# Kernel tuning notes

Hardware: AMD Instinct MI355X
Metric: run time of the kernel (lower is better)

Reference implementation:

```python
import jax, jax.numpy as jnp
import numpy as np

DIM = 1024
TOPK = 64
PAIRS = DIM // 2  # phase_pairs default
PHASE_MIX = 0.5
GATE_THRESHOLD = 0.0
EPS = 1e-12  # F.normalize default eps


def _l2norm(v):
    # matches F.normalize(v, dim=-1): v / max(||v||, eps)
    n = jnp.linalg.norm(v, axis=-1, keepdims=True)
    return v / jnp.maximum(n, EPS)


def setup_inputs() -> dict:
    key = jax.random.key(0)
    ks = jax.random.split(key, 6)
    s = 0.02  # small init scale for weights
    return {
        "x": jax.random.normal(ks[0], (4, 4096, DIM), dtype=jnp.float32),
        "gate_W": jax.random.normal(ks[1], (DIM, DIM), dtype=jnp.float32) * s,
        "gate_b": jnp.zeros((DIM,), dtype=jnp.float32),
        "mag_W": jax.random.normal(ks[2], (DIM, DIM), dtype=jnp.float32) * s,
        "mag_b": jnp.zeros((DIM,), dtype=jnp.float32),
        "Wq": jax.random.normal(ks[3], (DIM, DIM), dtype=jnp.float32) * s,
        "Wk": jax.random.normal(ks[4], (DIM, DIM), dtype=jnp.float32) * s,
        "phase_W": jax.random.normal(ks[5], (2 * PAIRS, DIM), dtype=jnp.float32) * s,
    }


def reference(x, gate_W, gate_b, mag_W, mag_b, Wq, Wk, phase_W):
    B, S, D = x.shape
    # gated SAE-style projection (gated=True, diag=False)
    gate_pre = x @ gate_W.T + gate_b          # [B,S,D]
    mag_pre = x @ mag_W.T + mag_b             # [B,S,D]
    # hard gate with straight-through estimator
    gate_soft = jax.nn.sigmoid(gate_pre)
    gate_hard = (gate_pre > GATE_THRESHOLD).astype(x.dtype)
    gate = gate_hard + gate_soft - jax.lax.stop_gradient(gate_soft)
    mag = jax.nn.relu(mag_pre)
    # top-k scatter mask along feature dim
    idx = jax.lax.top_k(gate_pre, TOPK)[1]    # [B,S,K]
    rows = jnp.arange(B * S)[:, None]
    mask = (jnp.zeros((B * S, D), dtype=bool)
            .at[rows, idx.reshape(B * S, TOPK)].set(True)
            .reshape(B, S, D))
    gate = jnp.where(mask, gate, jnp.zeros_like(gate))
    mag = jnp.where(mask, mag, jnp.zeros_like(mag))
    xg = gate * mag
    # twist projections, L2-normalized
    q = _l2norm(xg @ Wq.T)
    k = _l2norm(xg @ Wk.T)
    # symplectic momentum map over consecutive steps
    momentum_map = q[:, 1:] * k[:, :-1] - q[:, :-1] * k[:, 1:]  # [B,S-1,D]
    twist_mag = jnp.linalg.norm(momentum_map, axis=-1, keepdims=True)
    complexity = jnp.pad(jnp.tanh(twist_mag), ((0, 0), (1, 0), (0, 0)))  # [B,S,1]
    # phase branch (phase_mix > 0)
    phase = (xg @ phase_W.T).reshape(B, S, PAIRS, 2)
    phase = _l2norm(phase)
    pp, pc = phase[:, :-1], phase[:, 1:]
    cross = pp[..., 0] * pc[..., 1] - pp[..., 1] * pc[..., 0]   # [B,S-1,P]
    dot = jnp.clip(jnp.sum(pp * pc, axis=-1), -1.0, 1.0)
    phase_delta = jnp.abs(jnp.arctan2(cross, dot)) / jnp.pi
    phase_score = jnp.pad(jnp.mean(phase_delta, axis=-1, keepdims=True),
                          ((0, 0), (1, 0), (0, 0)))             # [B,S,1]
    return (1.0 - PHASE_MIX) * complexity + PHASE_MIX * phase_score
```

## Files before the change

### kernel.cpp

```cpp
#include <hip/hip_runtime.h>
#include <math.h>

#define DIM 1024
#define ROWS 16384
#define SEQ 4096
#define MARGIN 0.012f
#define MAXC 24

typedef __bf16 v8bf __attribute__((ext_vector_type(8)));
typedef float v4f __attribute__((ext_vector_type(4)));
typedef int v8i __attribute__((ext_vector_type(8)));

__device__ __forceinline__ unsigned short f2bf(float f){
  unsigned u = __float_as_uint(f);
  u = u + 0x7FFFu + ((u >> 16) & 1u);
  return (unsigned short)(u >> 16);
}
__device__ __forceinline__ float bf2f(unsigned short h){
  return __uint_as_float(((unsigned)h) << 16);
}
__device__ __forceinline__ unsigned short relu_bf(unsigned short h){
  return (h & 0x8000u) ? (unsigned short)0 : h;
}
__device__ __forceinline__ unsigned f2fp8(float f){
  float a = fabsf(f);
  unsigned sign = (__float_as_uint(f) >> 24) & 0x80u;
  if (a >= 448.f) return sign | 0x7Eu;
  if (a < 0.015625f){
    int k = (int)rintf(a * 512.f);
    if (k >= 8) return sign | 0x08u;
    return sign | (unsigned)k;
  }
  unsigned u = __float_as_uint(a);
  u += 0x7FFFFu + ((u >> 20) & 1u);
  int e = (int)((u >> 23) & 0xFFu) - 127;
  unsigned m = (u >> 20) & 7u;
  if (e > 8) return sign | 0x7Eu;
  return sign | ((unsigned)(e + 7) << 3) | m;
}
__device__ __forceinline__ void lds_fence(){
  __asm__ volatile("s_waitcnt lgkmcnt(0)" ::: "memory");
}

__global__ __launch_bounds__(256) void cvt_all(
    const float* __restrict__ x,
    const float* __restrict__ w0, const float* __restrict__ w1,
    const float* __restrict__ w2, const float* __restrict__ w3,
    const float* __restrict__ w4,
    unsigned short* __restrict__ xbf, unsigned short* __restrict__ wbf,
    unsigned char* __restrict__ wf8){
  const int y = blockIdx.y;
  int i = (blockIdx.x * 256 + threadIdx.x) * 4;
  if (y < 16){
    const float* s = x + ((size_t)y << 20);
    float4 f = *(const float4*)(s + i);
    ushort4 o; o.x = f2bf(f.x); o.y = f2bf(f.y); o.z = f2bf(f.z); o.w = f2bf(f.w);
    *(ushort4*)(xbf + ((size_t)y << 20) + i) = o;
  } else if (y < 18){
    const float* s = (y == 16) ? w0 : w1;
    float4 f = *(const float4*)(s + i);
    ushort4 o; o.x = f2bf(f.x); o.y = f2bf(f.y); o.z = f2bf(f.z); o.w = f2bf(f.w);
    *(ushort4*)(wbf + ((size_t)(y - 16) << 20) + i) = o;
  } else {
    const float* s = (y == 18) ? w2 : ((y == 19) ? w3 : w4);
    float4 f = *(const float4*)(s + i);
    unsigned u = f2fp8(f.x * 32.f) | (f2fp8(f.y * 32.f) << 8) |
                 (f2fp8(f.z * 32.f) << 16) | (f2fp8(f.w * 32.f) << 24);
    *(unsigned*)(wf8 + ((size_t)(y - 18) << 20) + i) = u;
  }
}

#define GBAR() asm volatile("s_barrier" ::: "memory")
#define GLGKM0() { asm volatile("s_waitcnt lgkmcnt(0)" ::: "memory"); __builtin_amdgcn_sched_barrier(0); }
#define GVM4() asm volatile("s_waitcnt vmcnt(4)" ::: "memory")

__global__ __launch_bounds__(512, 2) void gemm_bt(
    const unsigned short* __restrict__ A, const unsigned short* __restrict__ B,
    const float* __restrict__ bias0, const float* __restrict__ bias1,
    unsigned short* __restrict__ C0, unsigned short* __restrict__ C1)
{
  extern __shared__ unsigned char lds[];
  const int t = threadIdx.x;
  const int lane = t & 63, wave = t >> 6;
  const int wr = wave >> 2, wc = wave & 3;
  const int bid = blockIdx.x;
  const int swz = (bid & 7) * 64 + (bid >> 3);
  const int m0 = (swz & 63) * 256;
  const int n0 = (swz >> 6) * 256;

  int offv[4];
#pragma unroll
  for (int h = 0; h < 2; h++)
#pragma unroll
    for (int i = 0; i < 2; i++){
      int o = h * 16384 + i * 8192 + t * 16;
      int u = o ^ (((o >> 9) & 1) << 5);
      int r = ((u >> 11) << 4) | ((u >> 6) & 15);
      int c = (((u >> 10) & 1) << 5) | ((u & 63) >> 1);
      offv[h * 2 + i] = r * 1024 + c;
    }
  const int off00 = offv[0], off01 = offv[1], off10 = offv[2], off11 = offv[3];
  const unsigned short* Ab = A + ((size_t)m0 << 10);
  const unsigned short* Bb = B + ((size_t)n0 << 10);

  const int laneterm = (lane & 15) * 64 + (((lane >> 4) * 16) ^ (((lane >> 3) & 1) * 32));
  const int aBase = wr * 16384 + laneterm;
  const int bBase = 32768 + wc * 8192 + laneterm;

#define GLD1(srcp, dsto) __builtin_amdgcn_global_load_lds( \
    (const __attribute__((address_space(1))) void*)(srcp), \
    (__attribute__((address_space(3))) void*)(lds + (dsto)), 16, 0, 0)

  auto stageA = [&](int h, int kt, int pp){
    const int o0 = h ? off10 : off00, o1 = h ? off11 : off01;
    GLD1(Ab + o0 + kt * 64, pp * 65536 + h * 16384 + t * 16);
    GLD1(Ab + o1 + kt * 64, pp * 65536 + h * 16384 + 8192 + t * 16);
  };
  auto stageB = [&](int h, int kt, int pp){
    const int o0 = h ? off10 : off00, o1 = h ? off11 : off01;
    GLD1(Bb + o0 + kt * 64, pp * 65536 + 32768 + h * 16384 + t * 16);
    GLD1(Bb + o1 + kt * 64, pp * 65536 + 32768 + h * 16384 + 8192 + t * 16);
  };

  v4f acc[8][4];
#pragma unroll
  for (int i = 0; i < 8; i++)
#pragma unroll
    for (int j = 0; j < 4; j++) acc[i][j] = v4f{0.f, 0.f, 0.f, 0.f};

  stageB(0, 0, 0); stageB(1, 0, 0);
  stageA(0, 0, 0); stageA(1, 0, 0);
  stageB(0, 1, 1); stageB(1, 1, 1);
  GVM4();
  GBAR();

  int p = 0;
  for (int X = 0; X < 16; X++, p ^= 1){
    const int pb = p * 65536;
    const int ktA = (X + 1 < 16) ? X + 1 : 15;
    const int ktB = (X + 2 < 16) ? X + 2 : X;
    v8bf a0[8], a1[8], b0[4], b1[4];

#pragma unroll
    for (int mi = 0; mi < 8; mi++) a0[mi] = *(const v8bf*)(lds + pb + aBase + mi * 2048);
#pragma unroll
    for (int ni = 0; ni < 4; ni++) b0[ni] = *(const v8bf*)(lds + pb + bBase + ni * 2048);
    stageA(0, ktA, p ^ 1);
    GBAR();
    __builtin_amdgcn_s_setprio(1);
#pragma unroll
    for (int mi = 0; mi < 4; mi++)
#pragma unroll
      for (int ni = 0; ni < 4; ni++)
        acc[mi][ni] = __builtin_amdgcn_mfma_f32_16x16x32_bf16(a0[mi], b0[ni], acc[mi][ni], 0, 0, 0);
    __builtin_amdgcn_s_setprio(0);
    GBAR();

#pragma unroll
    for (int mi = 0; mi < 4; mi++) a1[mi] = *(const v8bf*)(lds + pb + aBase + 1024 + mi * 2048);
#pragma unroll
    for (int ni = 0; ni < 4; ni++) b1[ni] = *(const v8bf*)(lds + pb + bBase + 1024 + ni * 2048);
    stageA(1, ktA, p ^ 1);
    GBAR();
    __builtin_amdgcn_s_setprio(1);
#pragma unroll
    for (int mi = 0; mi < 4; mi++)
#pragma unroll
      for (int ni = 0; ni < 4; ni++)
        acc[4 + mi][ni] = __builtin_amdgcn_mfma_f32_16x16x32_bf16(a0[4 + mi], b0[ni], acc[4 + mi][ni], 0, 0, 0);
    __builtin_amdgcn_s_setprio(0);
    GLGKM0();
    GBAR();

#pragma unroll
    for (int mi = 4; mi < 8; mi++) a1[mi] = *(const v8bf*)(lds + pb + aBase + 1024 + mi * 2048);
    stageB(0, ktB, p);
    GBAR();
    __builtin_amdgcn_s_setprio(1);
#pragma unroll
    for (int mi = 0; mi < 4; mi++)
#pragma unroll
      for (int ni = 0; ni < 4; ni++)
        acc[mi][ni] = __builtin_amdgcn_mfma_f32_16x16x32_bf16(a1[mi], b1[ni], acc[mi][ni], 0, 0, 0);
    __builtin_amdgcn_s_setprio(0);
    GBAR();

    stageB(1, ktB, p);
    GBAR();
    __builtin_amdgcn_s_setprio(1);
#pragma unroll
    for (int mi = 0; mi < 4; mi++)
#pragma unroll
      for (int ni = 0; ni < 4; ni++)
        acc[4 + mi][ni] = __builtin_amdgcn_mfma_f32_16x16x32_bf16(a1[4 + mi], b1[ni], acc[4 + mi][ni], 0, 0, 0);
    __builtin_amdgcn_s_setprio(0);
    GVM4();
    GBAR();
  }

  asm volatile("s_waitcnt vmcnt(0)" ::: "memory");
  __syncthreads();

  const int os = n0 >> 10;
  unsigned short* Cp = (os == 0) ? C0 : C1;
  const float* bp = (os == 0) ? bias0 : bias1;
  const int colbase = n0 & (DIM - 1);
  unsigned short* lt = (unsigned short*)lds;
  const int ar = lane & 15, aq = lane >> 4;
  const int lrw = wr * 16 + aq * 4;
  const int lrow = t >> 4;
  const int cseg = (t & 15) * 16;
  const size_t grb = (size_t)(m0 + (lrow >> 4) * 128 + (lrow & 15)) * DIM + colbase + cseg;
  float bv[4];
#pragma unroll
  for (int ni = 0; ni < 4; ni++) bv[ni] = bp[colbase + wc * 64 + ni * 16 + ar];
#pragma unroll
  for (int mi = 0; mi < 8; mi++){
#pragma unroll
    for (int ni = 0; ni < 4; ni++){
      const int colc = wc * 64 + ni * 16 + ar;
#pragma unroll
      for (int rr = 0; rr < 4; rr++)
        lt[(lrw + rr) * 264 + colc] = f2bf(acc[mi][ni][rr] + bv[ni]);
    }
    __syncthreads();
    uint4 v0 = *(const uint4*)&lt[lrow * 264 + cseg];
    uint4 v1 = *(const uint4*)&lt[lrow * 264 + cseg + 8];
    *(uint4*)(Cp + grb + (size_t)mi * 16 * DIM) = v0;
    *(uint4*)(Cp + grb + (size_t)mi * 16 * DIM + 8) = v1;
    __syncthreads();
  }
  asm volatile("s_waitcnt vmcnt(0)" ::: "memory");
}

__global__ __launch_bounds__(256, 3) void gemm8(
    const unsigned char* __restrict__ A, const unsigned char* __restrict__ B,
    unsigned short* __restrict__ C0, unsigned short* __restrict__ C1,
    unsigned short* __restrict__ C2)
{
  __shared__ unsigned char lA[128 * 128];
  __shared__ unsigned char lB[128 * 128];
  const int t = threadIdx.x;
  const int lane = t & 63, wave = t >> 6;
  const int bid0 = blockIdx.y * gridDim.x + blockIdx.x;
  const int swz = (bid0 & 7) * 384 + (bid0 >> 3);
  const int m0 = (swz & 127) * 128;
  const int n0 = (swz >> 7) * 128;
  const int wm = (wave >> 1) * 64, wn = (wave & 1) * 64;
  const int ar = lane & 15, aq = lane >> 4;

  v4f acc[4][4];
#pragma unroll
  for (int i = 0; i < 4; i++)
#pragma unroll
    for (int j = 0; j < 4; j++) acc[i][j] = v4f{0.f, 0.f, 0.f, 0.f};

  for (int k0 = 0; k0 < DIM; k0 += 128){
#pragma unroll
    for (int i = 0; i < 4; i++){
      int c = (wave * 4 + i) * 64 + lane;
      int row = c >> 3, kq = c & 7;
      __builtin_amdgcn_global_load_lds(
        (const __attribute__((address_space(1))) void*)(A + (size_t)(m0 + row) * DIM + k0 + kq * 16),
        (__attribute__((address_space(3))) void*)(&lA[c * 16]), 16, 0, 0);
      __builtin_amdgcn_global_load_lds(
        (const __attribute__((address_space(1))) void*)(B + (size_t)(n0 + row) * DIM + k0 + kq * 16),
        (__attribute__((address_space(3))) void*)(&lB[c * 16]), 16, 0, 0);
    }
    __syncthreads();
    v8i a8[4], b8[4];
#pragma unroll
    for (int i = 0; i < 4; i++){
      a8[i] = *(const v8i*)&lA[(wm + i * 16 + ar) * 128 + aq * 32];
      b8[i] = *(const v8i*)&lB[(wn + i * 16 + ar) * 128 + aq * 32];
    }
#pragma unroll
    for (int mi = 0; mi < 4; mi++)
#pragma unroll
      for (int ni = 0; ni < 4; ni++)
        acc[mi][ni] = __builtin_amdgcn_mfma_scale_f32_16x16x128_f8f6f4(
            a8[mi], b8[ni], acc[mi][ni], 0, 0, 0, 127u, 0, 127u);
    __syncthreads();
  }

  const int os = n0 >> 10;
  unsigned short* Cp = (os == 0) ? C0 : ((os == 1) ? C1 : C2);
  const int colbase = n0 & (DIM - 1);
  unsigned short* lt = (unsigned short*)lA;
  const int lrw = (wave >> 1) * 16 + aq * 4;
  const int colc0 = (wave & 1) * 64;
  const int lrow = t >> 3;
  const int cseg = (t & 7) * 16;
  const size_t grb = (size_t)(m0 + (lrow >> 4) * 64 + (lrow & 15)) * DIM + colbase + cseg;
#pragma unroll
  for (int mi = 0; mi < 4; mi++){
#pragma unroll
    for (int ni = 0; ni < 4; ni++){
      const int colc = colc0 + ni * 16 + ar;
#pragma unroll
      for (int rr = 0; rr < 4; rr++)
        lt[(lrw + rr) * 136 + colc] = f2bf(acc[mi][ni][rr] * 0.03125f);
    }
    __syncthreads();
    uint4 v0 = *(const uint4*)&lt[lrow * 136 + cseg];
    uint4 v1 = *(const uint4*)&lt[lrow * 136 + cseg + 8];
    *(uint4*)(Cp + grb + (size_t)mi * 16 * DIM) = v0;
    *(uint4*)(Cp + grb + (size_t)mi * 16 * DIM + 8) = v1;
    __syncthreads();
  }
}

__global__ __launch_bounds__(256) void select_k(
  const unsigned short* __restrict__ gate_pre, const unsigned short* __restrict__ mag_pre,
  const float* __restrict__ x, const float* __restrict__ gW, const float* __restrict__ gb,
  unsigned char* __restrict__ xg8)
{
  __shared__ int   s_h  [4][256];
  __shared__ int   s_cnt[4];
  __shared__ int   s_idx[4][MAXC];
  __shared__ float s_ex [4][MAXC];
  __shared__ int   s_res[4][MAXC];

  const int t = threadIdx.x;
  const int lane = t & 63, wave = t >> 6;
  const int row = blockIdx.x * 4 + wave;
  const size_t rb = (size_t)row * DIM;

  uint4 ga = *(const uint4*)(gate_pre + rb + lane * 8);
  uint4 gB = *(const uint4*)(gate_pre + rb + 512 + lane * 8);
  float4 xa0 = *(const float4*)(x + rb + lane * 8);
  float4 xa1 = *(const float4*)(x + rb + lane * 8 + 4);
  float4 xb0 = *(const float4*)(x + rb + 512 + lane * 8);
  float4 xb1 = *(const float4*)(x + rb + 512 + lane * 8 + 4);
  uint4 ma = *(const uint4*)(mag_pre + rb + lane * 8);
  uint4 mb = *(const uint4*)(mag_pre + rb + 512 + lane * 8);

  unsigned gw[8] = {ga.x, ga.y, ga.z, ga.w, gB.x, gB.y, gB.z, gB.w};
  unsigned mw[8] = {ma.x, ma.y, ma.z, ma.w, mb.x, mb.y, mb.z, mb.w};
  float vg[16], vm[16];
  unsigned kk[16];
#pragma unroll
  for (int j = 0; j < 8; j++){
    unsigned w = gw[j];
    vg[2*j]   = __uint_as_float(w << 16);
    vg[2*j+1] = __uint_as_float(w & 0xFFFF0000u);
    unsigned lo = w & 0xFFFFu, hi = w >> 16;
    kk[2*j]   = (lo & 0x8000u) ? (~lo & 0xFFFFu) : (lo | 0x8000u);
    kk[2*j+1] = (hi & 0x8000u) ? (~hi & 0xFFFFu) : (hi | 0x8000u);
    unsigned m = mw[j];
    vm[2*j]   = __uint_as_float(m << 16);
    vm[2*j+1] = __uint_as_float(m & 0xFFFF0000u);
  }
  float vx[16] = {xa0.x, xa0.y, xa0.z, xa0.w, xa1.x, xa1.y, xa1.z, xa1.w,
                  xb0.x, xb0.y, xb0.z, xb0.w, xb1.x, xb1.y, xb1.z, xb1.w};

  if (lane == 0) s_cnt[wave] = 0;

  auto findbin = [&](int rk, int &bout, int &Cout){
    int c0 = s_h[wave][lane*4+0], c1 = s_h[wave][lane*4+1];
    int c2 = s_h[wave][lane*4+2], c3 = s_h[wave][lane*4+3];
    int sl = c0 + c1 + c2 + c3;
    int tt = sl;
#pragma unroll
    for (int m = 1; m < 64; m <<= 1){
      int u = __shfl(tt, lane + m);
      if (lane + m < 64) tt += u;
    }
    int ab = tt - sl;
    int bb = -1, CC = 0;
    int a3 = ab;       if (a3 < rk && rk <= a3 + c3){ bb = lane*4+3; CC = a3; }
    int a2 = ab + c3;  if (bb < 0 && a2 < rk && rk <= a2 + c2){ bb = lane*4+2; CC = a2; }
    int a1 = a2 + c2;  if (bb < 0 && a1 < rk && rk <= a1 + c1){ bb = lane*4+1; CC = a1; }
    int a0 = a1 + c1;  if (bb < 0 && a0 < rk && rk <= a0 + c0){ bb = lane*4+0; CC = a0; }
    unsigned long long mk = __ballot(bb >= 0);
    int src = (int)__ffsll(mk) - 1;
    bout = __shfl(bb, src); Cout = __shfl(CC, src);
  };

  s_h[wave][lane*4+0] = 0; s_h[wave][lane*4+1] = 0;
  s_h[wave][lane*4+2] = 0; s_h[wave][lane*4+3] = 0;
  lds_fence();
#pragma unroll
  for (int e = 0; e < 16; e++) atomicAdd(&s_h[wave][kk[e] >> 8], 1);
  lds_fence();
  int b1, C1; findbin(64, b1, C1);

  s_h[wave][lane*4+0] = 0; s_h[wave][lane*4+1] = 0;
  s_h[wave][lane*4+2] = 0; s_h[wave][lane*4+3] = 0;
  lds_fence();
#pragma unroll
  for (int e = 0; e < 16; e++)
    if ((int)(kk[e] >> 8) == b1) atomicAdd(&s_h[wave][kk[e] & 255u], 1);
  lds_fence();
  int b2, C2; findbin(64 - C1, b2, C2);

  unsigned tkey = ((unsigned)b1 << 8) | (unsigned)b2;
  unsigned hthr = (tkey & 0x8000u) ? (tkey & 0x7FFFu) : (~tkey & 0xFFFFu);
  const float thr = bf2f((unsigned short)hthr);
  const float cl = thr - MARGIN, ch = thr + MARGIN;

  int n1 = 0;
#pragma unroll
  for (int e = 0; e < 16; e++) n1 += (vg[e] > ch) ? 1 : 0;
#pragma unroll
  for (int m = 32; m; m >>= 1) n1 += __shfl_xor(n1, m);
  const int s = 64 - n1;

  lds_fence();
#pragma unroll
  for (int e = 0; e < 16; e++){
    float vv = vg[e];
    if (vv >= cl && vv <= ch){
      int p = atomicAdd(&s_cnt[wave], 1);
      if (p < MAXC) s_idx[wave][p] = (e >> 3) * 512 + lane * 8 + (e & 7);
    }
  }
  lds_fence();
  int namb = s_cnt[wave]; if (namb > MAXC) namb = MAXC;

  const int o0 = lane * 8, o1 = lane * 8 + 4, o2 = 512 + lane * 8, o3 = 512 + lane * 8 + 4;
  float4 w0, w1, w2, w3;
  int dcur = 0;
  if (namb > 0){
    dcur = s_idx[wave][0];
    const float* wr0 = gW + (size_t)dcur * DIM;
    w0 = *(const float4*)(wr0 + o0); w1 = *(const float4*)(wr0 + o1);
    w2 = *(const float4*)(wr0 + o2); w3 = *(const float4*)(wr0 + o3);
  }
  for (int i = 0; i < namb; i++){
    float4 c0 = w0, c1 = w1, c2 = w2, c3 = w3;
    int dn = 0;
    if (i + 1 < namb){
      dn = s_idx[wave][i + 1];
      const float* wr2 = gW + (size_t)dn * DIM;
      w0 = *(const float4*)(wr2 + o0); w1 = *(const float4*)(wr2 + o1);
      w2 = *(const float4*)(wr2 + o2); w3 = *(const float4*)(wr2 + o3);
    }
    float p = 0.f;
    p = fmaf(vx[0], c0.x, p);  p = fmaf(vx[1], c0.y, p);
    p = fmaf(vx[2], c0.z, p);  p = fmaf(vx[3], c0.w, p);
    p = fmaf(vx[4], c1.x, p);  p = fmaf(vx[5], c1.y, p);
    p = fmaf(vx[6], c1.z, p);  p = fmaf(vx[7], c1.w, p);
    p = fmaf(vx[8], c2.x, p);  p = fmaf(vx[9], c2.y, p);
    p = fmaf(vx[10], c2.z, p); p = fmaf(vx[11], c2.w, p);
    p = fmaf(vx[12], c3.x, p); p = fmaf(vx[13], c3.y, p);
    p = fmaf(vx[14], c3.z, p); p = fmaf(vx[15], c3.w, p);
#pragma unroll
    for (int m = 32; m; m >>= 1) p += __shfl_xor(p, m);
    if (lane == 0) s_ex[wave][i] = p + gb[dcur];
    dcur = dn;
  }
  lds_fence();

  if (lane < namb){
    float e = s_ex[wave][lane]; int d = s_idx[wave][lane];
    int rank = 0;
    for (int j = 0; j < namb; j++){
      float ej = s_ex[wave][j]; int dj = s_idx[wave][j];
      if (ej > e || (ej == e && dj < d)) rank++;
    }
    s_res[wave][lane] = (rank < s && e > 0.f) ? 1 : 0;
  }
  lds_fence();

  unsigned inb = 0, rsm = 0;
  for (int i = 0; i < namb; i++){
    int d = s_idx[wave][i];
    if (((d & 511) >> 3) == lane){
      int e = (d >> 9) * 8 + (d & 7);
      inb |= 1u << e;
      if (s_res[wave][i]) rsm |= 1u << e;
    }
  }

  float vals[16];
#pragma unroll
  for (int e = 0; e < 16; e++){
    float mv = (vm[e] > 0.f) ? vm[e] : 0.f;
    float v = (vg[e] > ch && vg[e] > 0.f) ? mv : 0.f;
    if ((inb >> e) & 1u) v = ((rsm >> e) & 1u) ? mv : 0.f;
    vals[e] = v;
  }

  unsigned pk[4];
#pragma unroll
  for (int q = 0; q < 4; q++){
    unsigned a = 0, b = 0;
    asm volatile("v_cvt_pk_fp8_f32 %0, %1, %2" : "+v"(a) : "v"(vals[4*q+0]), "v"(vals[4*q+1]));
    asm volatile("v_cvt_pk_fp8_f32 %0, %1, %2" : "+v"(b) : "v"(vals[4*q+2]), "v"(vals[4*q+3]));
    pk[q] = (a & 0xFFFFu) | (b << 16);
  }
  uint2 st0; st0.x = pk[0]; st0.y = pk[1];
  uint2 st1; st1.x = pk[2]; st1.y = pk[3];
  *(uint2*)(xg8 + rb + lane * 8) = st0;
  *(uint2*)(xg8 + rb + 512 + lane * 8) = st1;
}

__global__ __launch_bounds__(256) void epilogue_k(
  const unsigned short* __restrict__ q_pre, const unsigned short* __restrict__ k_pre,
  const unsigned short* __restrict__ p_pre, float* __restrict__ out)
{
  const int r0 = blockIdx.x * 4;
  const int t = threadIdx.x;
  const int lane = t & 63, wave = t >> 6;
  __shared__ float red[16];

  const int rp = (r0 == 0) ? 0 : r0 - 1;
  float vqp[4], vkp[4], vpp[4];
  {
    ushort4 uq = *(const ushort4*)(q_pre + (size_t)rp * DIM + 4*t);
    ushort4 uk = *(const ushort4*)(k_pre + (size_t)rp * DIM + 4*t);
    ushort4 up = *(const ushort4*)(p_pre + (size_t)rp * DIM + 4*t);
    vqp[0]=bf2f(uq.x); vqp[1]=bf2f(uq.y); vqp[2]=bf2f(uq.z); vqp[3]=bf2f(uq.w);
    vkp[0]=bf2f(uk.x); vkp[1]=bf2f(uk.y); vkp[2]=bf2f(uk.z); vkp[3]=bf2f(uk.w);
    vpp[0]=bf2f(up.x); vpp[1]=bf2f(up.y); vpp[2]=bf2f(up.z); vpp[3]=bf2f(up.w);
  }
  float aq = 0.f, ak = 0.f;
#pragma unroll
  for (int j = 0; j < 4; j++){ aq = fmaf(vqp[j], vqp[j], aq); ak = fmaf(vkp[j], vkp[j], ak); }
#pragma unroll
  for (int m = 32; m; m >>= 1){ aq += __shfl_xor(aq, m); ak += __shfl_xor(ak, m); }
  if (lane == 0){ red[wave] = aq; red[4 + wave] = ak; }
  __syncthreads();
  float rqp = 1.f / fmaxf(sqrtf(red[0] + red[1] + red[2] + red[3]), 1e-12f);
  float rkp = 1.f / fmaxf(sqrtf(red[4] + red[5] + red[6] + red[7]), 1e-12f);
  __syncthreads();

  for (int rr = 0; rr < 4; rr++){
    const int r = r0 + rr;
    float vqc[4], vkc[4], vpc[4];
    {
      ushort4 uq = *(const ushort4*)(q_pre + (size_t)r * DIM + 4*t);
      ushort4 uk = *(const ushort4*)(k_pre + (size_t)r * DIM + 4*t);
      ushort4 up = *(const ushort4*)(p_pre + (size_t)r * DIM + 4*t);
      vqc[0]=bf2f(uq.x); vqc[1]=bf2f(uq.y); vqc[2]=bf2f(uq.z); vqc[3]=bf2f(uq.w);
      vkc[0]=bf2f(uk.x); vkc[1]=bf2f(uk.y); vkc[2]=bf2f(uk.z); vkc[3]=bf2f(uk.w);
      vpc[0]=bf2f(up.x); vpc[1]=bf2f(up.y); vpc[2]=bf2f(up.z); vpc[3]=bf2f(up.w);
    }
    const bool seg = (r & (SEQ - 1)) == 0;
    float aqc = 0.f, akc = 0.f;
#pragma unroll
    for (int j = 0; j < 4; j++){ aqc = fmaf(vqc[j], vqc[j], aqc); akc = fmaf(vkc[j], vkc[j], akc); }
    float dsum = 0.f;
    if (!seg){
#pragma unroll
      for (int j = 0; j < 2; j++){
        float ax = vpp[2*j], ay = vpp[2*j+1], bx = vpc[2*j], by = vpc[2*j+1];
        float ia = 1.f / fmaxf(sqrtf(ax * ax + ay * ay), 1e-12f);
        float ib = 1.f / fmaxf(sqrtf(bx * bx + by * by), 1e-12f);
        ax *= ia; ay *= ia; bx *= ib; by *= ib;
        float cross = ax * by - ay * bx;
        float dot = fminf(fmaxf(ax * bx + ay * by, -1.f), 1.f);
        dsum += fabsf(atan2f(cross, dot)) * 0.3183098861837907f;
      }
    }
#pragma unroll
    for (int m = 32; m; m >>= 1){
      aqc += __shfl_xor(aqc, m); akc += __shfl_xor(akc, m); dsum += __shfl_xor(dsum, m);
    }
    if (lane == 0){ red[wave] = aqc; red[4 + wave] = akc; red[8 + wave] = dsum; }
    __syncthreads();
    float rqc = 1.f / fmaxf(sqrtf(red[0] + red[1] + red[2] + red[3]), 1e-12f);
    float rkc = 1.f / fmaxf(sqrtf(red[4] + red[5] + red[6] + red[7]), 1e-12f);
    if (!seg){
      float tw = 0.f;
#pragma unroll
      for (int j = 0; j < 4; j++){
        float m = (vqc[j] * rqc) * (vkp[j] * rkp) - (vqp[j] * rqp) * (vkc[j] * rkc);
        tw = fmaf(m, m, tw);
      }
#pragma unroll
      for (int m = 32; m; m >>= 1) tw += __shfl_xor(tw, m);
      if (lane == 0) red[12 + wave] = tw;
      __syncthreads();
      if (t == 0){
        float dtot = red[8] + red[9] + red[10] + red[11];
        float twt = red[12] + red[13] + red[14] + red[15];
        out[r] = 0.5f * tanhf(sqrtf(twt)) + 0.5f * (dtot * (1.f / 512.f));
      }
    } else {
      if (t == 0) out[r] = 0.f;
    }
    __syncthreads();
#pragma unroll
    for (int j = 0; j < 4; j++){ vqp[j] = vqc[j]; vkp[j] = vkc[j]; vpp[j] = vpc[j]; }
    rqp = rqc; rkp = rkc;
  }
}

extern "C" void kernel_launch(void* const* d_in, const int* in_sizes, int n_in,
                              void* d_out, int out_size, void* d_ws, size_t ws_size,
                              hipStream_t stream)
{
  const float* x       = (const float*)d_in[0];
  const float* gate_W  = (const float*)d_in[1];
  const float* gate_b  = (const float*)d_in[2];
  const float* mag_W   = (const float*)d_in[3];
  const float* mag_b   = (const float*)d_in[4];
  const float* Wq      = (const float*)d_in[5];
  const float* Wk      = (const float*)d_in[6];
  const float* phase_W = (const float*)d_in[7];
  float* out = (float*)d_out;

  char* ws = (char*)d_ws;
  unsigned short* xbf = (unsigned short*)ws;
  unsigned short* wbf = (unsigned short*)(ws + 33554432);
  unsigned char*  wf8 = (unsigned char*)(ws + 37748736);
  unsigned short* gate_pre = (unsigned short*)(ws + 41943040);
  unsigned short* mag_pre  = (unsigned short*)(ws + 75497472);
  unsigned short* p_pre    = (unsigned short*)(ws + 109051904);
  unsigned short* q_pre = gate_pre;
  unsigned short* k_pre = mag_pre;

  static bool attr_set = false;
  if (!attr_set){
    hipFuncSetAttribute((const void*)gemm_bt,
                        hipFuncAttributeMaxDynamicSharedMemorySize, 131072);
    attr_set = true;
  }

  dim3 b256(256);
  cvt_all<<<dim3(1024, 21), b256, 0, stream>>>(x, gate_W, mag_W, Wq, Wk, phase_W,
                                               xbf, wbf, wf8);

  gemm_bt<<<dim3(512), dim3(512), 131072, stream>>>(xbf, wbf, gate_b, mag_b,
                                                    gate_pre, mag_pre);

  unsigned char* xg8 = (unsigned char*)xbf;
  select_k<<<ROWS / 4, b256, 0, stream>>>(gate_pre, mag_pre, x, gate_W, gate_b, xg8);

  gemm8<<<dim3(24, 128), b256, 0, stream>>>(xg8, wf8, q_pre, k_pre, p_pre);

  epilogue_k<<<ROWS / 4, b256, 0, stream>>>(q_pre, k_pre, p_pre, out);
}
```

Measured before the change: 382.6 us.

## Restructure FP8 gemm8 into 256x256 tiles with double-buffered swizzled LDS pipeline

Rewrites the FP8 projection GEMM to use 512-thread blocks computing 256x256 output tiles. Operands are staged into 128KB of dynamic LDS with an XOR swizzle, and loads are double-buffered so the next K-slice's global-to-LDS copies overlap the MFMA work. Wave priority is raised around the MFMA blocks. The larger tiles and pipelining target the memory stalls and low reuse of the old 128x128 single-buffered loop, at the cost of more registers and LDS per block and lower occupancy.

```diff
diff --git a/kernel.cpp b/kernel.cpp
--- a/kernel.cpp
+++ b/kernel.cpp
@@ -233,77 +233,130 @@
   asm volatile("s_waitcnt vmcnt(0)" ::: "memory");
 }
 
-__global__ __launch_bounds__(256, 3) void gemm8(
+__global__ __launch_bounds__(512, 2) void gemm8(
     const unsigned char* __restrict__ A, const unsigned char* __restrict__ B,
     unsigned short* __restrict__ C0, unsigned short* __restrict__ C1,
     unsigned short* __restrict__ C2)
 {
-  __shared__ unsigned char lA[128 * 128];
-  __shared__ unsigned char lB[128 * 128];
+  extern __shared__ unsigned char lds[];
   const int t = threadIdx.x;
   const int lane = t & 63, wave = t >> 6;
-  const int bid0 = blockIdx.y * gridDim.x + blockIdx.x;
-  const int swz = (bid0 & 7) * 384 + (bid0 >> 3);
-  const int m0 = (swz & 127) * 128;
-  const int n0 = (swz >> 7) * 128;
-  const int wm = (wave >> 1) * 64, wn = (wave & 1) * 64;
+  const int wr = wave >> 2, wc = wave & 3;
+  const int bid = blockIdx.x;
+  const int swz = (bid & 7) * 96 + (bid >> 3);
+  const int m0 = (swz / 12) * 256;
+  const int n0 = (swz % 12) * 256;
+
+  int offv[4];
+#pragma unroll
+  for (int h = 0; h < 2; h++)
+#pragma unroll
+    for (int i = 0; i < 2; i++){
+      int d = h * 16384 + i * 8192 + t * 16;
+      int row = d >> 7;
+      int colg = (d & 127) ^ ((row & 7) << 4);
+      offv[h * 2 + i] = row * 1024 + colg;
+    }
+  const unsigned char* Ab = A + ((size_t)m0 << 10);
+  const unsigned char* Bb = B + ((size_t)n0 << 10);
+
   const int ar = lane & 15, aq = lane >> 4;
-
-  v4f acc[4][4];
-#pragma unroll
-  for (int i = 0; i < 4; i++)
+  const int lt0 = ar * 128 + ((aq * 32) ^ ((ar & 7) << 4));
+  const int lt1 = lt0 ^ 16;
+  const int aBase = wr * 16384;
+  const int bBase = 32768 + wc * 8192;
+
+  auto stageA8 = [&](int h, int kt, int pp){
+    GLD1(Ab + offv[h * 2 + 0] + kt * 128, pp * 65536 + h * 16384 + t * 16);
+    GLD1(Ab + offv[h * 2 + 1] + kt * 128, pp * 65536 + h * 16384 + 8192 + t * 16);
+  };
+  auto stageB8 = [&](int h, int kt, int pp){
+    GLD1(Bb + offv[h * 2 + 0] + kt * 128, pp * 65536 + 32768 + h * 16384 + t * 16);
+    GLD1(Bb + offv[h * 2 + 1] + kt * 128, pp * 65536 + 32768 + h * 16384 + 8192 + t * 16);
+  };
+  auto ldv8 = [&](int off) -> v8i {
+    int4 lo = *(const int4*)(lds + off);
+    int4 hi = *(const int4*)(lds + (off ^ 16));
+    v8i r; r[0]=lo.x; r[1]=lo.y; r[2]=lo.z; r[3]=lo.w;
+    r[4]=hi.x; r[5]=hi.y; r[6]=hi.z; r[7]=hi.w;
+    return r;
+  };
+
+  v4f acc[8][4];
+#pragma unroll
+  for (int i = 0; i < 8; i++)
 #pragma unroll
     for (int j = 0; j < 4; j++) acc[i][j] = v4f{0.f, 0.f, 0.f, 0.f};
 
-  for (int k0 = 0; k0 < DIM; k0 += 128){
-#pragma unroll
-    for (int i = 0; i < 4; i++){
-      int c = (wave * 4 + i) * 64 + lane;
-      int row = c >> 3, kq = c & 7;
-      __builtin_amdgcn_global_load_lds(
-        (const __attribute__((address_space(1))) void*)(A + (size_t)(m0 + row) * DIM + k0 + kq * 16),
-        (__attribute__((address_space(3))) void*)(&lA[c * 16]), 16, 0, 0);
-      __builtin_amdgcn_global_load_lds(
-        (const __attribute__((address_space(1))) void*)(B + (size_t)(n0 + row) * DIM + k0 + kq * 16),
-        (__attribute__((address_space(3))) void*)(&lB[c * 16]), 16, 0, 0);
-    }
-    __syncthreads();
-    v8i a8[4], b8[4];
-#pragma unroll
-    for (int i = 0; i < 4; i++){
-      a8[i] = *(const v8i*)&lA[(wm + i * 16 + ar) * 128 + aq * 32];
-      b8[i] = *(const v8i*)&lB[(wn + i * 16 + ar) * 128 + aq * 32];
-    }
+  stageB8(0, 0, 0); stageB8(1, 0, 0);
+  stageA8(0, 0, 0); stageA8(1, 0, 0);
+  stageB8(0, 1, 1); stageB8(1, 1, 1);
+  GVM4();
+  GBAR();
+
+  int p = 0;
+  for (int X = 0; X < 8; X++, p ^= 1){
+    const int pb = p * 65536;
+    const int ktA = (X + 1 < 8) ? X + 1 : 7;
+    const int ktB = (X + 2 < 8) ? X + 2 : X;
+    v8i a0[4], a1[4], b0[4];
+
+#pragma unroll
+    for (int ni = 0; ni < 4; ni++) b0[ni] = ldv8(pb + bBase + ni * 2048 + lt0);
+#pragma unroll
+    for (int mi = 0; mi < 4; mi++) a0[mi] = ldv8(pb + aBase + mi * 2048 + lt0);
+    stageA8(0, ktA, p ^ 1); stageA8(1, ktA, p ^ 1);
+    GBAR();
+    __builtin_amdgcn_s_setprio(1);
 #pragma unroll
     for (int mi = 0; mi < 4; mi++)
 #pragma unroll
       for (int ni = 0; ni < 4; ni++)
         acc[mi][ni] = __builtin_amdgcn_mfma_scale_f32_16x16x128_f8f6f4(
-            a8[mi], b8[ni], acc[mi][ni], 0, 0, 0, 127u, 0, 127u);
-    __syncthreads();
-  }
+            a0[mi], b0[ni], acc[mi][ni], 0, 0, 0, 127u, 0, 127u);
+    __builtin_amdgcn_s_setprio(0);
+    GBAR();
+
+#pragma unroll
+    for (int mi = 0; mi < 4; mi++) a1[mi] = ldv8(pb + aBase + (4 + mi) * 2048 + lt0);
+    GLGKM0();
+    stageB8(0, ktB, p); stageB8(1, ktB, p);
+    GBAR();
+    __builtin_amdgcn_s_setprio(1);
+#pragma unroll
+    for (int mi = 0; mi < 4; mi++)
+#pragma unroll
+      for (int ni = 0; ni < 4; ni++)
+        acc[4 + mi][ni] = __builtin_amdgcn_mfma_scale_f32_16x16x128_f8f6f4(
+            a1[mi], b0[ni], acc[4 + mi][ni], 0, 0, 0, 127u, 0, 127u);
+    __builtin_amdgcn_s_setprio(0);
+    GVM4();
+    GBAR();
+  }
+
+  asm volatile("s_waitcnt vmcnt(0)" ::: "memory");
+  __syncthreads();
 
   const int os = n0 >> 10;
   unsigned short* Cp = (os == 0) ? C0 : ((os == 1) ? C1 : C2);
   const int colbase = n0 & (DIM - 1);
-  unsigned short* lt = (unsigned short*)lA;
-  const int lrw = (wave >> 1) * 16 + aq * 4;
-  const int colc0 = (wave & 1) * 64;
-  const int lrow = t >> 3;
-  const int cseg = (t & 7) * 16;
-  const size_t grb = (size_t)(m0 + (lrow >> 4) * 64 + (lrow & 15)) * DIM + colbase + cseg;
-#pragma unroll
-  for (int mi = 0; mi < 4; mi++){
+  unsigned short* lt = (unsigned short*)lds;
+  const int lrw = wr * 16 + aq * 4;
+  const int lrow = t >> 4;
+  const int cseg = (t & 15) * 16;
+  const size_t grb = (size_t)(m0 + (lrow >> 4) * 128 + (lrow & 15)) * DIM + colbase + cseg;
+#pragma unroll
+  for (int mi = 0; mi < 8; mi++){
 #pragma unroll
     for (int ni = 0; ni < 4; ni++){
-      const int colc = colc0 + ni * 16 + ar;
+      const int colc = wc * 64 + ni * 16 + ar;
 #pragma unroll
       for (int rr = 0; rr < 4; rr++)
-        lt[(lrw + rr) * 136 + colc] = f2bf(acc[mi][ni][rr] * 0.03125f);
+        lt[(lrw + rr) * 264 + colc] = f2bf(acc[mi][ni][rr] * 0.03125f);
     }
     __syncthreads();
-    uint4 v0 = *(const uint4*)&lt[lrow * 136 + cseg];
-    uint4 v1 = *(const uint4*)&lt[lrow * 136 + cseg + 8];
+    uint4 v0 = *(const uint4*)&lt[lrow * 264 + cseg];
+    uint4 v1 = *(const uint4*)&lt[lrow * 264 + cseg + 8];
     *(uint4*)(Cp + grb + (size_t)mi * 16 * DIM) = v0;
     *(uint4*)(Cp + grb + (size_t)mi * 16 * DIM + 8) = v1;
     __syncthreads();
@@ -616,6 +669,8 @@
   if (!attr_set){
     hipFuncSetAttribute((const void*)gemm_bt,
                         hipFuncAttributeMaxDynamicSharedMemorySize, 131072);
+    hipFuncSetAttribute((const void*)gemm8,
+                        hipFuncAttributeMaxDynamicSharedMemorySize, 131072);
     attr_set = true;
   }
 
@@ -629,7 +684,7 @@
   unsigned char* xg8 = (unsigned char*)xbf;
   select_k<<<ROWS / 4, b256, 0, stream>>>(gate_pre, mag_pre, x, gate_W, gate_b, xg8);
 
-  gemm8<<<dim3(24, 128), b256, 0, stream>>>(xg8, wf8, q_pre, k_pre, p_pre);
+  gemm8<<<dim3(768), dim3(512), 131072, stream>>>(xg8, wf8, q_pre, k_pre, p_pre);
 
   epilogue_k<<<ROWS / 4, b256, 0, stream>>>(q_pre, k_pre, p_pre, out);
 }
```

Result: no change. 379.0 us (-1.0%).

## Software-pipeline FP8 GEMM with register-direct A loads and swizzled multi-buffered B

Applied to the files above, without the earlier changes.

Rewrites the FP8 projection GEMM main loop. The A operand is now loaded straight from global into registers with double buffering, and B is staged into four swizzled LDS buffers with async global-to-LDS loads issued two k-tiles ahead. Barriers per k-step drop and the MFMA blocks run at raised wave priority, so memory latency is hidden behind compute. Occupancy drops from 3 to 2 blocks per CU because dynamic LDS grows to 64KB, and block-to-tile mapping changes to a 1D grid with a new swizzle.

```diff
diff --git a/kernel.cpp b/kernel.cpp
--- a/kernel.cpp
+++ b/kernel.cpp
@@ -73,6 +73,7 @@
 #define GBAR() asm volatile("s_barrier" ::: "memory")
 #define GLGKM0() { asm volatile("s_waitcnt lgkmcnt(0)" ::: "memory"); __builtin_amdgcn_sched_barrier(0); }
 #define GVM4() asm volatile("s_waitcnt vmcnt(4)" ::: "memory")
+#define GVM12() asm volatile("s_waitcnt vmcnt(12)" ::: "memory")
 
 __global__ __launch_bounds__(512, 2) void gemm_bt(
     const unsigned short* __restrict__ A, const unsigned short* __restrict__ B,
@@ -233,60 +234,121 @@
   asm volatile("s_waitcnt vmcnt(0)" ::: "memory");
 }
 
-__global__ __launch_bounds__(256, 3) void gemm8(
+__global__ __launch_bounds__(256, 2) void gemm8(
     const unsigned char* __restrict__ A, const unsigned char* __restrict__ B,
     unsigned short* __restrict__ C0, unsigned short* __restrict__ C1,
     unsigned short* __restrict__ C2)
 {
-  __shared__ unsigned char lA[128 * 128];
-  __shared__ unsigned char lB[128 * 128];
+  extern __shared__ unsigned char lds[];
   const int t = threadIdx.x;
   const int lane = t & 63, wave = t >> 6;
-  const int bid0 = blockIdx.y * gridDim.x + blockIdx.x;
-  const int swz = (bid0 & 7) * 384 + (bid0 >> 3);
-  const int m0 = (swz & 127) * 128;
-  const int n0 = (swz >> 7) * 128;
-  const int wm = (wave >> 1) * 64, wn = (wave & 1) * 64;
+  const int wm = (wave >> 1) * 64;
+  const int wn = (wave & 1) * 64;
   const int ar = lane & 15, aq = lane >> 4;
 
+  const int bid = blockIdx.x;
+  const int loc = bid >> 3;
+  const int m0 = ((bid & 7) * 16 + (loc & 15)) * 128;
+  const int n0 = (loc >> 4) * 128;
+
+  const unsigned char* Ab = A + ((size_t)m0 << 10);
+  const unsigned char* Bb = B + ((size_t)n0 << 10);
+
+  int offb[4];
+#pragma unroll
+  for (int i = 0; i < 4; i++){
+    int d = i * 4096 + t * 16;
+    int row = d >> 7;
+    offb[i] = row * 1024 + ((d & 127) ^ ((row & 7) << 4));
+  }
+  auto stageB = [&](int kt, int bi){
+#pragma unroll
+    for (int i = 0; i < 4; i++)
+      GLD1(Bb + offb[i] + kt * 128, bi * 16384 + i * 4096 + t * 16);
+  };
+
+  const unsigned char* Arow = Ab + (size_t)(wm + ar) * 1024 + aq * 32;
+  auto loadA = [&](int kt, int4 (&lo)[4], int4 (&hi)[4]){
+#pragma unroll
+    for (int mi = 0; mi < 4; mi++){
+      const unsigned char* p = Arow + mi * 16384 + kt * 128;
+      lo[mi] = *(const int4*)p;
+      hi[mi] = *(const int4*)(p + 16);
+    }
+  };
+
+  auto readB = [&](int bi, v8i (&bf)[4]){
+#pragma unroll
+    for (int ni = 0; ni < 4; ni++){
+      int r = wn + ni * 16 + ar;
+      int base = bi * 16384 + r * 128 + ((aq * 32) ^ ((r & 7) << 4));
+      int4 lo = *(const int4*)(lds + base);
+      int4 hi = *(const int4*)(lds + (base ^ 16));
+      v8i v; v[0]=lo.x; v[1]=lo.y; v[2]=lo.z; v[3]=lo.w;
+             v[4]=hi.x; v[5]=hi.y; v[6]=hi.z; v[7]=hi.w;
+      bf[ni] = v;
+    }
+  };
+
   v4f acc[4][4];
 #pragma unroll
   for (int i = 0; i < 4; i++)
 #pragma unroll
     for (int j = 0; j < 4; j++) acc[i][j] = v4f{0.f, 0.f, 0.f, 0.f};
 
-  for (int k0 = 0; k0 < DIM; k0 += 128){
-#pragma unroll
-    for (int i = 0; i < 4; i++){
-      int c = (wave * 4 + i) * 64 + lane;
-      int row = c >> 3, kq = c & 7;
-      __builtin_amdgcn_global_load_lds(
-        (const __attribute__((address_space(1))) void*)(A + (size_t)(m0 + row) * DIM + k0 + kq * 16),
-        (__attribute__((address_space(3))) void*)(&lA[c * 16]), 16, 0, 0);
-      __builtin_amdgcn_global_load_lds(
-        (const __attribute__((address_space(1))) void*)(B + (size_t)(n0 + row) * DIM + k0 + kq * 16),
-        (__attribute__((address_space(3))) void*)(&lB[c * 16]), 16, 0, 0);
-    }
-    __syncthreads();
-    v8i a8[4], b8[4];
-#pragma unroll
-    for (int i = 0; i < 4; i++){
-      a8[i] = *(const v8i*)&lA[(wm + i * 16 + ar) * 128 + aq * 32];
-      b8[i] = *(const v8i*)&lB[(wn + i * 16 + ar) * 128 + aq * 32];
-    }
-#pragma unroll
-    for (int mi = 0; mi < 4; mi++)
+  auto domfma = [&](int4 (&lo)[4], int4 (&hi)[4], v8i (&bf)[4]){
+    __builtin_amdgcn_s_setprio(1);
+#pragma unroll
+    for (int mi = 0; mi < 4; mi++){
+      v8i a; a[0]=lo[mi].x; a[1]=lo[mi].y; a[2]=lo[mi].z; a[3]=lo[mi].w;
+             a[4]=hi[mi].x; a[5]=hi[mi].y; a[6]=hi[mi].z; a[7]=hi[mi].w;
 #pragma unroll
       for (int ni = 0; ni < 4; ni++)
         acc[mi][ni] = __builtin_amdgcn_mfma_scale_f32_16x16x128_f8f6f4(
-            a8[mi], b8[ni], acc[mi][ni], 0, 0, 0, 127u, 0, 127u);
-    __syncthreads();
-  }
-
+            a, bf[ni], acc[mi][ni], 0, 0, 0, 127u, 0, 127u);
+    }
+    __builtin_amdgcn_s_setprio(0);
+  };
+
+  int4 eL[4], eH[4], oL[4], oH[4];
+
+  stageB(0, 0); stageB(1, 1);
+  loadA(0, eL, eH);
+  GVM12();
+  GBAR();
+
+  for (int j = 0; j < 4; j++){
+    const int X = 2 * j;
+    const int pj = j & 1;
+    const int rb0 = pj * 2, rb1 = rb0 + 1;
+    const int sb0 = (pj ^ 1) * 2, sb1 = sb0 + 1;
+    const int ktB2 = (X + 2 < 8) ? X + 2 : X;
+    const int ktB3 = (X + 3 < 8) ? X + 3 : X + 1;
+    const int ktA2 = (X + 2 < 8) ? X + 2 : 7;
+    v8i bf[4];
+
+    loadA(X + 1, oL, oH);
+    readB(rb0, bf);
+    GLGKM0();
+    stageB(ktB2, sb0);
+    domfma(eL, eH, bf);
+
+    loadA(ktA2, eL, eH);
+    GVM12();
+    readB(rb1, bf);
+    GLGKM0();
+    stageB(ktB3, sb1);
+    domfma(oL, oH, bf);
+    GVM12();
+    GBAR();
+  }
+
+  asm volatile("s_waitcnt vmcnt(0)" ::: "memory");
+  __syncthreads();
   const int os = n0 >> 10;
   unsigned short* Cp = (os == 0) ? C0 : ((os == 1) ? C1 : C2);
   const int colbase = n0 & (DIM - 1);
-  unsigned short* lt = (unsigned short*)lA;
+  unsigned short* lt = (unsigned short*)lds;
   const int lrw = (wave >> 1) * 16 + aq * 4;
   const int colc0 = (wave & 1) * 64;
   const int lrow = t >> 3;
@@ -616,6 +678,8 @@
   if (!attr_set){
     hipFuncSetAttribute((const void*)gemm_bt,
                         hipFuncAttributeMaxDynamicSharedMemorySize, 131072);
+    hipFuncSetAttribute((const void*)gemm8,
+                        hipFuncAttributeMaxDynamicSharedMemorySize, 65536);
     attr_set = true;
   }
 
@@ -629,7 +693,7 @@
   unsigned char* xg8 = (unsigned char*)xbf;
   select_k<<<ROWS / 4, b256, 0, stream>>>(gate_pre, mag_pre, x, gate_W, gate_b, xg8);
 
-  gemm8<<<dim3(24, 128), b256, 0, stream>>>(xg8, wf8, q_pre, k_pre, p_pre);
+  gemm8<<<dim3(3072), b256, 65536, stream>>>(xg8, wf8, q_pre, k_pre, p_pre);
 
   epilogue_k<<<ROWS / 4, b256, 0, stream>>>(q_pre, k_pre, p_pre, out);
 }
```

Measured after the change: 483.0 us. 26.2% more time.
